# Performance work log

Hardware: AMD Instinct MI355X
Metric: run time of the kernel (lower is better)

The kernel has to match this reference:

```python
import jax, jax.numpy as jnp
import numpy as np

VAR0, VAR1 = 0.1, 0.2
CONF_THR = 0.02
NMS_THR = 0.4
PRE_K = 5000
POST_K = 750
N = 85680


def setup_inputs() -> dict:
    key = jax.random.key(0)
    k0, k1, k2, k3 = jax.random.split(key, 4)
    return {
        "loc": jax.random.normal(k0, (N, 4), jnp.float32),
        "conf": jax.random.uniform(k1, (N, 2), jnp.float32),
        "landmarks": jax.random.normal(k2, (N, 10), jnp.float32),
        "priors": jax.random.uniform(k3, (N, 4), jnp.float32),
        "img_w": 1920,
        "img_h": 1088,
    }


def _decode_boxes(loc, priors):
    # center-size decode -> xyxy
    cxy = priors[:, :2] + loc[:, :2] * VAR0 * priors[:, 2:]
    wh = priors[:, 2:] * jnp.exp(loc[:, 2:] * VAR1)
    return jnp.concatenate([cxy - wh * 0.5, cxy + wh * 0.5], axis=-1)


def _decode_landmarks(lmk, priors):
    pts = lmk.reshape(-1, 5, 2)                       # [N,5,2]
    out = priors[:, None, :2] + pts * VAR0 * priors[:, None, 2:]
    return out.reshape(-1, 10)


def _pairwise_iou(boxes):
    # boxes: [K,4] xyxy
    area = (boxes[:, 2] - boxes[:, 0]) * (boxes[:, 3] - boxes[:, 1])
    lt = jnp.maximum(boxes[:, None, :2], boxes[None, :, :2])  # [K,K,2]
    rb = jnp.minimum(boxes[:, None, 2:], boxes[None, :, 2:])
    wh = jnp.clip(rb - lt, 0.0)
    inter = wh[..., 0] * wh[..., 1]
    union = area[:, None] + area[None, :] - inter
    return inter / jnp.maximum(union, 1e-12)


def _greedy_nms(boxes, valid, thr):
    # boxes already sorted by descending score; valid marks real candidates.
    K = boxes.shape[0]
    iou = _pairwise_iou(boxes)                         # [K,K]
    idx = jnp.arange(K)

    def body(i, keep):
        suppress = keep[i] & (iou[i] > thr) & (idx > i)
        return keep & ~suppress

    return jax.lax.fori_loop(0, K, body, valid)


def reference(loc, conf, landmarks, priors, img_w, img_h):
    w = jnp.float32(img_w)
    h = jnp.float32(img_h)
    bbox_scale = jnp.array([w, h, w, h], jnp.float32)
    lmk_scale = jnp.tile(jnp.array([w, h], jnp.float32), 5)

    boxes = _decode_boxes(loc, priors) * bbox_scale          # [N,4]
    lmk = _decode_landmarks(landmarks, priors) * lmk_scale   # [N,10]
    scores = conf[:, 1]                                      # [N]

    # confidence filter fused into top-k via -inf masking (static shapes)
    masked = jnp.where(scores > CONF_THR, scores, -jnp.inf)
    top_scores, order = jax.lax.top_k(masked, PRE_K)         # [PRE_K]
    boxes_k = boxes[order]
    lmk_k = lmk[order]
    valid_k = top_scores > CONF_THR

    keep = _greedy_nms(boxes_k, valid_k, NMS_THR)            # [PRE_K] bool

    # compact kept rows (already score-sorted) into fixed [POST_K,15]
    rank = jnp.cumsum(keep) - 1
    rows = jnp.concatenate([boxes_k, top_scores[:, None], lmk_k], axis=1)
    dest = jnp.where(keep & (rank < POST_K), rank, POST_K)   # OOB -> dropped
    out = jnp.zeros((POST_K, 15), jnp.float32).at[dest].set(rows, mode="drop")
    return out
```

## Files before the change

kernel.cpp:

```cpp
#include <hip/hip_runtime.h>
#include <hip/hip_bf16.h>
#include <math.h>

#define N_IN 85680
#define PRE_K 5000
#define POST_K 750
#define NW 79
#define NPAD 5056
#define HSIZE 8192
#define CAND_MAX 8192
#define CONF_THR 0.02f
#define NMS_THR 0.4f
#define BITS_THR 0x3CA3D70Bu

typedef unsigned int u32;
typedef unsigned long long u64;

__device__ __forceinline__ int cbase(int k) { return k * (5088 - 32 * k); }

__device__ __forceinline__ float opaquef(float x) { asm volatile("" : "+v"(x)); return x; }

__device__ __forceinline__ u32 bucket_of(u32 bits) {
    u32 b = (bits - BITS_THR) >> 13;
    return b >= HSIZE ? (HSIZE - 1) : b;
}

__global__ __launch_bounds__(256) void hist_kernel(const float2* __restrict__ conf2,
                                                   u32* __restrict__ hist) {
    __shared__ u32 h[HSIZE];
    for (int b = threadIdx.x; b < HSIZE; b += 256) h[b] = 0u;
    __syncthreads();
    int i = blockIdx.x * 256 + threadIdx.x;
    if (i < N_IN) {
        float s = conf2[i].y;
        if (s > CONF_THR) atomicAdd(&h[bucket_of(__float_as_uint(s))], 1u);
    }
    __syncthreads();
    for (int b = threadIdx.x; b < HSIZE; b += 256) {
        u32 v = h[b];
        if (v) atomicAdd(&hist[b], v);
    }
}

__global__ __launch_bounds__(1024) void scan_kernel(const u32* __restrict__ hist,
                                                    u32* __restrict__ bsel,
                                                    u32* __restrict__ bstart) {
    __shared__ u32 tot[1024];
    int c = threadIdx.x;
    u32 lh[8];
    u32 t = 0;
#pragma unroll
    for (int k = 0; k < 8; ++k) { lh[k] = hist[c * 8 + k]; t += lh[k]; }
    tot[c] = t;
    __syncthreads();
    for (int d = 1; d < 1024; d <<= 1) {
        u32 v = tot[c] + ((c + d < 1024) ? tot[c + d] : 0u);
        __syncthreads();
        tot[c] = v;
        __syncthreads();
    }
    u32 above = (c + 1 < 1024) ? tot[c + 1] : 0u;
    u32 s = above;
    for (int k = 7; k >= 0; --k) { bstart[c * 8 + k] = s; s += lh[k]; }
    if (above < PRE_K && above + t >= PRE_K) {
        u32 cum = above;
        for (int k = 7; k >= 0; --k) {
            cum += lh[k];
            if (cum >= PRE_K) { bsel[0] = (u32)(c * 8 + k); break; }
        }
    }
    if (c == 0 && tot[0] < PRE_K) bsel[0] = 0u;
}

__global__ __launch_bounds__(256) void compact_kernel(const float2* __restrict__ conf2,
                                                      const u32* __restrict__ bsel,
                                                      const u32* __restrict__ bstart,
                                                      u32* __restrict__ bfill,
                                                      u64* __restrict__ cand) {
    int i = blockIdx.x * 256 + threadIdx.x;
    if (i >= N_IN) return;
    float sc = conf2[i].y;
    if (!(sc > CONF_THR)) return;
    u32 bits = __float_as_uint(sc);
    u32 b = bucket_of(bits);
    if (b < bsel[0]) return;
    u32 pos = bstart[b] + atomicAdd(&bfill[b], 1u);
    if (pos < CAND_MAX) cand[pos] = ((u64)bits << 32) | (u64)(u32)(~(u32)i);
}

__global__ __launch_bounds__(256) void rankdec_kernel(const u64* __restrict__ cand,
                                                      const u32* __restrict__ bstart,
                                                      const u32* __restrict__ bfill,
                                                      const u32* __restrict__ bsel,
                                                      const float4* __restrict__ loc4,
                                                      const float4* __restrict__ pri4,
                                                      const float* __restrict__ lmk,
                                                      const int* __restrict__ imw,
                                                      const int* __restrict__ imh,
                                                      float4* __restrict__ rows4,
                                                      float4* __restrict__ boxes,
                                                      u64* __restrict__ validm) {
    u32 bs = bsel[0];
    u32 total = bstart[bs] + bfill[bs];
    if (total > CAND_MAX) total = CAND_MAX;
    float W = (float)(*imw), H = (float)(*imh);
    for (u32 s = blockIdx.x * blockDim.x + threadIdx.x; s < total;
         s += gridDim.x * blockDim.x) {
        u64 key = cand[s];
        u32 b = bucket_of((u32)(key >> 32));
        u32 st = bstart[b];
        u32 en = st + bfill[b];
        if (en > CAND_MAX) en = CAND_MAX;
        u32 r = st;
        for (u32 j = st; j < en; ++j) r += (cand[j] > key) ? 1u : 0u;
        if (r >= PRE_K) continue;
        u32 i = ~(u32)key;
        float score = __uint_as_float((u32)(key >> 32));
        float4 L = loc4[i];
        float4 P = pri4[i];
        float cx = P.x + opaquef((L.x * 0.1f) * P.z);
        float cy = P.y + opaquef((L.y * 0.1f) * P.w);
        float bw = P.z * (float)exp((double)(L.z * 0.2f));
        float bh = P.w * (float)exp((double)(L.w * 0.2f));
        float hw = opaquef(bw * 0.5f), hh = opaquef(bh * 0.5f);
        float x0 = (cx - hw) * W, y0 = (cy - hh) * H;
        float x1 = (cx + hw) * W, y1 = (cy + hh) * H;
        boxes[r] = make_float4(x0, y0, x1, y1);
        float lm[10];
#pragma unroll
        for (int p = 0; p < 5; ++p) {
            float2 q = ((const float2*)lmk)[(size_t)i * 5 + p];
            lm[2 * p]     = (P.x + opaquef((q.x * 0.1f) * P.z)) * W;
            lm[2 * p + 1] = (P.y + opaquef((q.y * 0.1f) * P.w)) * H;
        }
        float4* row = rows4 + (size_t)r * 4;
        row[0] = make_float4(x0, y0, x1, y1);
        row[1] = make_float4(score, lm[0], lm[1], lm[2]);
        row[2] = make_float4(lm[3], lm[4], lm[5], lm[6]);
        row[3] = make_float4(lm[7], lm[8], lm[9], 0.f);
        atomicOr(&validm[r >> 6], 1ull << (r & 63));
    }
}

__global__ __launch_bounds__(64) void mask_kernel(const float4* __restrict__ boxes,
                                                  u64* __restrict__ cmask) {
    int rem = blockIdx.x, rc = 0;
    while (rem >= rc + 1) { rem -= rc + 1; ++rc; }
    int cc = rem;
    __shared__ float4 cb[64];
    int t = threadIdx.x;
    cb[t] = boxes[cc * 64 + t];
    int i = rc * 64 + t;
    float4 bi = boxes[i];
    __syncthreads();
    float areai = (bi.z - bi.x) * (bi.w - bi.y);
    u64 word = 0ull;
#pragma unroll 4
    for (int k = 0; k < 64; ++k) {
        float4 bj = cb[k];
        float areaj = (bj.z - bj.x) * (bj.w - bj.y);
        float ltx = fmaxf(bi.x, bj.x), lty = fmaxf(bi.y, bj.y);
        float rbx = fminf(bi.z, bj.z), rby = fminf(bi.w, bj.w);
        float wx = fmaxf(rbx - ltx, 0.f), wy = fmaxf(rby - lty, 0.f);
        float inter = opaquef(wx * wy);
        float uni = fmaxf(areai + areaj - inter, 1e-12f);
        float iou = inter / uni;
        if (iou > NMS_THR) word |= (1ull << k);
    }
    if (i < PRE_K) cmask[(size_t)(cbase(cc) + (i - 64 * cc))] = word;
}

#define LDCOL(j, base, cnt) \
    (((j) < (cnt)) ? cmask[(size_t)(cbase((base) + (j)) + r - 64 * ((base) + (j)))] : 0ull)

#define WAITCNT(need)                                                                  \
    for (;;) {                                                                         \
        u32 d_ = __hip_atomic_load(&doneCnt, __ATOMIC_RELAXED,                         \
                                   __HIP_MEMORY_SCOPE_WORKGROUP);                      \
        if (d_ > (u32)NW) { dead = true; break; }                                      \
        if (d_ >= (u32)(need)) break;                                                  \
    }                                                                                  \
    asm volatile("" ::: "memory");

__global__ __launch_bounds__(512) void reduce_scatter_kernel(const u64* __restrict__ cmask,
                                                             const u64* __restrict__ validm,
                                                             const float* __restrict__ rows,
                                                             float* __restrict__ out) {
    int tid = threadIdx.x;
    int g = tid >> 6, lane = tid & 63;
    __shared__ u64 keepAll[96];
    __shared__ u32 totKs[96];
    __shared__ u32 doneCnt;
    __shared__ u32 wpref[96];
    for (int k = tid; k < 96; k += 512) keepAll[k] = 0ull;
    if (tid == 0) doneCnt = 0u;
    __syncthreads();
    u64 lmask = (1ull << lane) - 1ull;

    for (int s = 0; s < 10; ++s) {
        int w = s * 8 + g;
        if (w >= NW) break;
        int r = 64 * w + lane;
        u64 dlow = cmask[(size_t)(cbase(w) + lane)] & lmask;
        u64 dA = (w >= 1) ? cmask[(size_t)(cbase(w - 1) + r - 64 * (w - 1))] : 0ull;
        u64 dB = (w >= 2) ? cmask[(size_t)(cbase(w - 2) + r - 64 * (w - 2))] : 0ull;
        u64 valw = validm[w];
        int wcap = (w >= 2) ? (w - 2) : 0;
        u64 sup = 0ull;
        bool dead = false;

        int d0 = 0;
        int nb = wcap < 8 ? wcap : 8;
        u64 c0 = LDCOL(0, 0, nb), c1 = LDCOL(1, 0, nb), c2 = LDCOL(2, 0, nb), c3 = LDCOL(3, 0, nb);
        u64 c4 = LDCOL(4, 0, nb), c5 = LDCOL(5, 0, nb), c6 = LDCOL(6, 0, nb), c7 = LDCOL(7, 0, nb);
        while (d0 < wcap) {
            int d1 = d0 + nb;
            int nb2 = wcap - d1; if (nb2 > 8) nb2 = 8;
            u64 n0 = LDCOL(0, d1, nb2), n1 = LDCOL(1, d1, nb2), n2 = LDCOL(2, d1, nb2), n3 = LDCOL(3, d1, nb2);
            u64 n4 = LDCOL(4, d1, nb2), n5 = LDCOL(5, d1, nb2), n6 = LDCOL(6, d1, nb2), n7 = LDCOL(7, d1, nb2);
            WAITCNT(d0 + nb)
            if (dead) break;
            if (0 < nb) sup |= keepAll[d0 + 0] & c0;
            if (1 < nb) sup |= keepAll[d0 + 1] & c1;
            if (2 < nb) sup |= keepAll[d0 + 2] & c2;
            if (3 < nb) sup |= keepAll[d0 + 3] & c3;
            if (4 < nb) sup |= keepAll[d0 + 4] & c4;
            if (5 < nb) sup |= keepAll[d0 + 5] & c5;
            if (6 < nb) sup |= keepAll[d0 + 6] & c6;
            if (7 < nb) sup |= keepAll[d0 + 7] & c7;
            c0 = n0; c1 = n1; c2 = n2; c3 = n3; c4 = n4; c5 = n5; c6 = n6; c7 = n7;
            d0 = d1; nb = nb2;
        }
        if (!dead && w > 0) { WAITCNT(w) }
        u64 keep = 0ull;
        u32 tp = 0u;
        if (!dead) {
            tp = (w > 0) ? totKs[w - 1] : 0u;
            if (tp < POST_K) {
                if (w >= 2) sup |= keepAll[w - 2] & dB;
                if (w >= 1) sup |= keepAll[w - 1] & dA;
                keep = valw & ~__ballot(sup != 0ull);
                for (;;) {
                    bool con = (dlow & keep) != 0ull;
                    u64 cm = __ballot(con) & keep;
                    if (cm == 0ull) break;
                    keep &= ~(cm & (~cm + 1ull));
                }
            }
            if (lane == 0) {
                u32 tk = tp + (u32)__popcll(keep);
                keepAll[w] = keep;
                totKs[w] = tk;
                asm volatile("s_waitcnt lgkmcnt(0)" ::: "memory");
                __hip_atomic_store(&doneCnt,
                                   (tk >= POST_K) ? (u32)(NW + 9) : (u32)(w + 1),
                                   __ATOMIC_RELAXED, __HIP_MEMORY_SCOPE_WORKGROUP);
            }
        }
    }
    __syncthreads();

    if (tid == 0) {
        u32 s = 0;
        for (int w = 0; w < NW; ++w) { wpref[w] = s; s += (u32)__popcll(keepAll[w]); }
        wpref[NW] = s;
    }
    __syncthreads();
    u32 totk = wpref[NW]; if (totk > POST_K) totk = POST_K;
    for (int r = tid; r < PRE_K; r += 512) {
        int w = r >> 6, b = r & 63;
        u64 kw = keepAll[w];
        if ((kw >> b) & 1ull) {
            u32 rank = wpref[w] + (u32)__popcll(kw & ((1ull << b) - 1ull));
            if (rank < POST_K) {
                const float* src = rows + (size_t)r * 16;
                float* dst = out + (size_t)rank * 15;
#pragma unroll
                for (int c2 = 0; c2 < 15; ++c2) dst[c2] = src[c2];
            }
        }
    }
    for (int r = (int)totk + tid; r < POST_K; r += 512) {
        float* dst = out + (size_t)r * 15;
#pragma unroll
        for (int c2 = 0; c2 < 15; ++c2) dst[c2] = 0.f;
    }
}

extern "C" void kernel_launch(void* const* d_in, const int* in_sizes, int n_in,
                              void* d_out, int out_size, void* d_ws, size_t ws_size,
                              hipStream_t stream) {
    const float* loc = (const float*)d_in[0];
    const float2* conf2 = (const float2*)d_in[1];
    const float* lmk = (const float*)d_in[2];
    const float* pri = (const float*)d_in[3];
    const int* imw = (const int*)d_in[4];
    const int* imh = (const int*)d_in[5];
    float* out = (float*)d_out;
    char* base = (char*)d_ws;

    u32* hist   = (u32*)(base + 0);
    u32* bfill  = (u32*)(base + 32768);
    u32* bsel   = (u32*)(base + 65536);
    u64* validm = (u64*)(base + 65600);
    u32* bstart = (u32*)(base + 67648);
    u64* cand   = (u64*)(base + 100416);
    float* rows = (float*)(base + 165952);
    float4* boxes = (float4*)(base + 485952);
    u64* cmask  = (u64*)(base + 566848);

    hipMemsetAsync(d_ws, 0, 66624, stream);

    hist_kernel<<<(N_IN + 255) / 256, 256, 0, stream>>>(conf2, hist);
    scan_kernel<<<1, 1024, 0, stream>>>(hist, bsel, bstart);
    compact_kernel<<<(N_IN + 255) / 256, 256, 0, stream>>>(conf2, bsel, bstart, bfill, cand);
    rankdec_kernel<<<24, 256, 0, stream>>>(cand, bstart, bfill, bsel, (const float4*)loc,
                                           (const float4*)pri, lmk, imw, imh,
                                           (float4*)rows, boxes, validm);
    mask_kernel<<<NW * (NW + 1) / 2, 64, 0, stream>>>(boxes, cmask);
    reduce_scatter_kernel<<<1, 512, 0, stream>>>(cmask, validm, rows, out);
}
```

Baseline: 110.9 us.

## Process NMS keep-mask words in groups of four per wave with faster intra-word solve

Result: faster. 94.78 us (-14.5%).

```diff
diff --git a/kernel.cpp b/kernel.cpp
--- a/kernel.cpp
+++ b/kernel.cpp
@@ -12,6 +12,7 @@
 #define CONF_THR 0.02f
 #define NMS_THR 0.4f
 #define BITS_THR 0x3CA3D70Bu
+#define NGRP 20
 
 typedef unsigned int u32;
 typedef unsigned long long u64;
@@ -170,17 +171,29 @@
     if (i < PRE_K) cmask[(size_t)(cbase(cc) + (i - 64 * cc))] = word;
 }
 
-#define LDCOL(j, base, cnt) \
-    (((j) < (cnt)) ? cmask[(size_t)(cbase((base) + (j)) + r - 64 * ((base) + (j)))] : 0ull)
-
-#define WAITCNT(need)                                                                  \
-    for (;;) {                                                                         \
-        u32 d_ = __hip_atomic_load(&doneCnt, __ATOMIC_RELAXED,                         \
-                                   __HIP_MEMORY_SCOPE_WORKGROUP);                      \
-        if (d_ > (u32)NW) { dead = true; break; }                                      \
-        if (d_ >= (u32)(need)) break;                                                  \
-    }                                                                                  \
+#define FC(k, q) cmask[(size_t)(cbase(k) + (q) - 64 * (k))]
+
+#define WAITG(need)                                                                   \
+    for (;;) {                                                                        \
+        u32 d_ = __hip_atomic_load(&doneCnt, __ATOMIC_RELAXED,                        \
+                                   __HIP_MEMORY_SCOPE_WORKGROUP);                     \
+        if (d_ > (u32)NGRP) { dead = true; break; }                                   \
+        if (d_ >= (u32)(need)) break;                                                 \
+    }                                                                                 \
     asm volatile("" ::: "memory");
+
+__device__ __forceinline__ u64 nms_solve(u64 valw, u64 sup, u64 dlow) {
+    u64 keep = valw & ~__ballot(sup != 0ull);
+    for (;;) {
+        u64 conm = __ballot((dlow & keep) != 0ull);
+        u64 cm = conm & keep;
+        if (cm == 0ull) break;
+        u64 U = keep & ~conm;
+        u64 rem = __ballot((dlow & U) != 0ull) & keep;
+        keep &= ~rem;
+    }
+    return keep;
+}
 
 __global__ __launch_bounds__(512) void reduce_scatter_kernel(const u64* __restrict__ cmask,
                                                              const u64* __restrict__ validm,
@@ -189,7 +202,7 @@
     int tid = threadIdx.x;
     int g = tid >> 6, lane = tid & 63;
     __shared__ u64 keepAll[96];
-    __shared__ u32 totKs[96];
+    __shared__ u32 totG[32];
     __shared__ u32 doneCnt;
     __shared__ u32 wpref[96];
     for (int k = tid; k < 96; k += 512) keepAll[k] = 0ull;
@@ -197,65 +210,83 @@
     __syncthreads();
     u64 lmask = (1ull << lane) - 1ull;
 
-    for (int s = 0; s < 10; ++s) {
-        int w = s * 8 + g;
-        if (w >= NW) break;
-        int r = 64 * w + lane;
-        u64 dlow = cmask[(size_t)(cbase(w) + lane)] & lmask;
-        u64 dA = (w >= 1) ? cmask[(size_t)(cbase(w - 1) + r - 64 * (w - 1))] : 0ull;
-        u64 dB = (w >= 2) ? cmask[(size_t)(cbase(w - 2) + r - 64 * (w - 2))] : 0ull;
-        u64 valw = validm[w];
-        int wcap = (w >= 2) ? (w - 2) : 0;
-        u64 sup = 0ull;
+    for (int s = 0; s < 3; ++s) {
+        int G = s * 8 + g;
+        if (G >= NGRP) break;
+        int w0 = 4 * G;
+        int nwg = NW - w0; if (nwg > 4) nwg = 4;
+        int q0 = 64 * w0 + lane;
+        int q1 = q0 + 64;
+        int q2 = q0 + 128;
+        int q3 = (nwg > 3) ? (q0 + 192) : q0;
+        u64 t00 = FC(w0, q0);
+        u64 t10 = (nwg > 1) ? FC(w0, q1) : 0ull;
+        u64 t11 = (nwg > 1) ? FC(w0 + 1, q1) : 0ull;
+        u64 t20 = (nwg > 2) ? FC(w0, q2) : 0ull;
+        u64 t21 = (nwg > 2) ? FC(w0 + 1, q2) : 0ull;
+        u64 t22 = (nwg > 2) ? FC(w0 + 2, q2) : 0ull;
+        u64 t30 = (nwg > 3) ? FC(w0, q3) : 0ull;
+        u64 t31 = (nwg > 3) ? FC(w0 + 1, q3) : 0ull;
+        u64 t32 = (nwg > 3) ? FC(w0 + 2, q3) : 0ull;
+        u64 t33 = (nwg > 3) ? FC(w0 + 3, q3) : 0ull;
+        u64 v0 = validm[w0];
+        u64 v1 = (nwg > 1) ? validm[w0 + 1] : 0ull;
+        u64 v2 = (nwg > 2) ? validm[w0 + 2] : 0ull;
+        u64 v3 = (nwg > 3) ? validm[w0 + 3] : 0ull;
+        u64 sup0 = 0, sup1 = 0, sup2 = 0, sup3 = 0;
         bool dead = false;
 
         int d0 = 0;
-        int nb = wcap < 8 ? wcap : 8;
-        u64 c0 = LDCOL(0, 0, nb), c1 = LDCOL(1, 0, nb), c2 = LDCOL(2, 0, nb), c3 = LDCOL(3, 0, nb);
-        u64 c4 = LDCOL(4, 0, nb), c5 = LDCOL(5, 0, nb), c6 = LDCOL(6, 0, nb), c7 = LDCOL(7, 0, nb);
-        while (d0 < wcap) {
-            int d1 = d0 + nb;
-            int nb2 = wcap - d1; if (nb2 > 8) nb2 = 8;
-            u64 n0 = LDCOL(0, d1, nb2), n1 = LDCOL(1, d1, nb2), n2 = LDCOL(2, d1, nb2), n3 = LDCOL(3, d1, nb2);
-            u64 n4 = LDCOL(4, d1, nb2), n5 = LDCOL(5, d1, nb2), n6 = LDCOL(6, d1, nb2), n7 = LDCOL(7, d1, nb2);
-            WAITCNT(d0 + nb)
+        u64 c00=0,c01=0,c02=0,c03=0,c10=0,c11=0,c12=0,c13=0;
+        if (w0 > 0) {
+            c00 = FC(0, q0); c01 = FC(0, q1); c02 = FC(0, q2); c03 = FC(0, q3);
+            c10 = FC(1, q0); c11 = FC(1, q1); c12 = FC(1, q2); c13 = FC(1, q3);
+        }
+        asm volatile("" ::: "memory");
+        while (d0 < w0) {
+            int d1 = d0 + 2;
+            u64 n00=0,n01=0,n02=0,n03=0,n10=0,n11=0,n12=0,n13=0;
+            if (d1 < w0) {
+                n00 = FC(d1, q0);     n01 = FC(d1, q1);     n02 = FC(d1, q2);     n03 = FC(d1, q3);
+                n10 = FC(d1 + 1, q0); n11 = FC(d1 + 1, q1); n12 = FC(d1 + 1, q2); n13 = FC(d1 + 1, q3);
+            }
+            asm volatile("" ::: "memory");
+            WAITG(((d0 + 1) >> 2) + 1)
             if (dead) break;
-            if (0 < nb) sup |= keepAll[d0 + 0] & c0;
-            if (1 < nb) sup |= keepAll[d0 + 1] & c1;
-            if (2 < nb) sup |= keepAll[d0 + 2] & c2;
-            if (3 < nb) sup |= keepAll[d0 + 3] & c3;
-            if (4 < nb) sup |= keepAll[d0 + 4] & c4;
-            if (5 < nb) sup |= keepAll[d0 + 5] & c5;
-            if (6 < nb) sup |= keepAll[d0 + 6] & c6;
-            if (7 < nb) sup |= keepAll[d0 + 7] & c7;
-            c0 = n0; c1 = n1; c2 = n2; c3 = n3; c4 = n4; c5 = n5; c6 = n6; c7 = n7;
-            d0 = d1; nb = nb2;
-        }
-        if (!dead && w > 0) { WAITCNT(w) }
-        u64 keep = 0ull;
-        u32 tp = 0u;
+            u64 ka = keepAll[d0], kb = keepAll[d0 + 1];
+            sup0 |= (ka & c00) | (kb & c10);
+            sup1 |= (ka & c01) | (kb & c11);
+            sup2 |= (ka & c02) | (kb & c12);
+            sup3 |= (ka & c03) | (kb & c13);
+            c00=n00;c01=n01;c02=n02;c03=n03;c10=n10;c11=n11;c12=n12;c13=n13;
+            d0 = d1;
+        }
         if (!dead) {
-            tp = (w > 0) ? totKs[w - 1] : 0u;
+            u32 tp = (G > 0) ? totG[G - 1] : 0u;
+            u64 k0 = 0, k1 = 0, k2 = 0, k3 = 0;
             if (tp < POST_K) {
-                if (w >= 2) sup |= keepAll[w - 2] & dB;
-                if (w >= 1) sup |= keepAll[w - 1] & dA;
-                keep = valw & ~__ballot(sup != 0ull);
-                for (;;) {
-                    bool con = (dlow & keep) != 0ull;
-                    u64 cm = __ballot(con) & keep;
-                    if (cm == 0ull) break;
-                    keep &= ~(cm & (~cm + 1ull));
-                }
+                k0 = nms_solve(v0, sup0, t00 & lmask);
+                sup1 |= k0 & t10; sup2 |= k0 & t20; sup3 |= k0 & t30;
+                k1 = nms_solve(v1, sup1, t11 & lmask);
+                sup2 |= k1 & t21; sup3 |= k1 & t31;
+                k2 = nms_solve(v2, sup2, t22 & lmask);
+                sup3 |= k2 & t32;
+                k3 = nms_solve(v3, sup3, t33 & lmask);
             }
             if (lane == 0) {
-                u32 tk = tp + (u32)__popcll(keep);
-                keepAll[w] = keep;
-                totKs[w] = tk;
+                keepAll[w0]     = k0;
+                keepAll[w0 + 1] = k1;
+                keepAll[w0 + 2] = k2;
+                keepAll[w0 + 3] = k3;
+                u32 tk = tp + (u32)(__popcll(k0) + __popcll(k1) + __popcll(k2) + __popcll(k3));
+                totG[G] = tk;
                 asm volatile("s_waitcnt lgkmcnt(0)" ::: "memory");
                 __hip_atomic_store(&doneCnt,
-                                   (tk >= POST_K) ? (u32)(NW + 9) : (u32)(w + 1),
+                                   (tk >= POST_K) ? (u32)(NGRP + 9) : (u32)(G + 1),
                                    __ATOMIC_RELAXED, __HIP_MEMORY_SCOPE_WORKGROUP);
             }
+        } else {
+            break;
         }
     }
     __syncthreads();
```
